# Kernel optimization log

Hardware: AMD Instinct MI355X
Metric: run time of the kernel (lower is better)

## Reference

```python
import jax, jax.numpy as jnp
import numpy as np

L, D, H, M, NC = 12, 768, 12, 3072, 1000
P, IMG, C = 16, 224, 3
HD = D // H // 2  # 32: diff-attn head dim (2*H query heads of HD, H value heads of 2*HD)
B = 32
N = (IMG // P) ** 2 + 1  # 197
EPS = 1e-5


def _layernorm(x, s, b):
    mu = x.mean(-1, keepdims=True)
    var = ((x - mu) ** 2).mean(-1, keepdims=True)
    return (x - mu) * jax.lax.rsqrt(var + EPS) * s + b


def _rmsnorm(x, s):
    ms = (x * x).mean(-1, keepdims=True)
    return x * jax.lax.rsqrt(ms + EPS) * s


def _diff_attn(x, qw, kw, vw, ow, lq1, lk1, lq2, lk2, sls, lam_init):
    b, n, _ = x.shape
    q = (x @ qw).reshape(b, n, 2 * H, HD)
    k = (x @ kw).reshape(b, n, 2 * H, HD)
    v = (x @ vw).reshape(b, n, H, 2 * HD)
    scores = jnp.einsum('bnhd,bmhd->bhnm', q, k) * (HD ** -0.5)
    attn = jax.nn.softmax(scores, axis=-1)  # [b, 2H, n, n]
    lam = jnp.exp(jnp.sum(lq1 * lk1)) - jnp.exp(jnp.sum(lq2 * lk2)) + lam_init
    attn = attn.reshape(b, H, 2, n, n)
    attn = attn[:, :, 0] - lam * attn[:, :, 1]  # differential attention map
    out = jnp.einsum('bhnm,bmhd->bnhd', attn, v)  # [b, n, H, 2*HD]
    out = _rmsnorm(out, sls) * (1.0 - lam_init)
    return out.reshape(b, n, D) @ ow


def _forward(x, conv_w, conv_b, cls_token, pos_emb,
             ln1_s, ln1_b, q_w, k_w, v_w, o_w, lq1, lk1, lq2, lk2, subln_s,
             ln2_s, ln2_b, w1, b1, w2, b2, lnf_s, lnf_b, head_w, head_b):
    # patch embed: conv stride=patch, then flatten to tokens
    h = jax.lax.conv_general_dilated(x, conv_w, (P, P), 'VALID',
                                     dimension_numbers=('NCHW', 'OIHW', 'NCHW'))
    h = h + conv_b[None, :, None, None]
    bsz = x.shape[0]
    h = h.reshape(bsz, D, -1).transpose(0, 2, 1)  # [B, 196, D]
    h = jnp.concatenate([jnp.broadcast_to(cls_token, (bsz, 1, D)), h], axis=1)
    h = h + pos_emb
    for i in range(L):
        lam_init = 0.8 - 0.6 * np.exp(-0.3 * i)
        a = _diff_attn(_layernorm(h, ln1_s[i], ln1_b[i]), q_w[i], k_w[i], v_w[i], o_w[i],
                       lq1[i], lk1[i], lq2[i], lk2[i], subln_s[i], lam_init)
        h = h + a
        m = _layernorm(h, ln2_s[i], ln2_b[i])
        m = jax.nn.gelu(m @ w1[i] + b1[i]) @ w2[i] + b2[i]
        h = h + m
    h = _layernorm(h, lnf_s, lnf_b)
    return h[:, 0] @ head_w + head_b


def setup_inputs() -> dict:
    key = jax.random.key(0)
    ks = iter(jax.random.split(key, 40))
    def rn(shape, s=0.02):
        return jax.random.normal(next(ks), shape, jnp.float32) * s
    return {
        'x': jax.random.normal(next(ks), (B, C, IMG, IMG), jnp.float32),
        'conv_w': rn((D, C, P, P)), 'conv_b': jnp.zeros((D,), jnp.float32),
        'cls_token': jnp.zeros((1, 1, D), jnp.float32),
        'pos_emb': rn((1, N, D)),
        'ln1_s': jnp.ones((L, D), jnp.float32), 'ln1_b': jnp.zeros((L, D), jnp.float32),
        'q_w': rn((L, D, D)), 'k_w': rn((L, D, D)), 'v_w': rn((L, D, D)), 'o_w': rn((L, D, D)),
        'lq1': rn((L, HD), 0.1), 'lk1': rn((L, HD), 0.1),
        'lq2': rn((L, HD), 0.1), 'lk2': rn((L, HD), 0.1),
        'subln_s': jnp.ones((L, 2 * HD), jnp.float32),
        'ln2_s': jnp.ones((L, D), jnp.float32), 'ln2_b': jnp.zeros((L, D), jnp.float32),
        'w1': rn((L, D, M)), 'b1': jnp.zeros((L, M), jnp.float32),
        'w2': rn((L, M, D)), 'b2': jnp.zeros((L, D), jnp.float32),
        'lnf_s': jnp.ones((D,), jnp.float32), 'lnf_b': jnp.zeros((D,), jnp.float32),
        'head_w': rn((D, NC)), 'head_b': jnp.zeros((NC,), jnp.float32),
    }


def reference(x, conv_w, conv_b, cls_token, pos_emb,
              ln1_s, ln1_b, q_w, k_w, v_w, o_w, lq1, lk1, lq2, lk2, subln_s,
              ln2_s, ln2_b, w1, b1, w2, b2, lnf_s, lnf_b, head_w, head_b):
    return _forward(x, conv_w, conv_b, cls_token, pos_emb,
                    ln1_s, ln1_b, q_w, k_w, v_w, o_w, lq1, lk1, lq2, lk2, subln_s,
                    ln2_s, ln2_b, w1, b1, w2, b2, lnf_s, lnf_b, head_w, head_b)
```

## Files before the change

kernel.cpp:

```cpp
#include <hip/hip_runtime.h>
#include <cmath>


typedef unsigned short u16;
typedef u16 u16x4 __attribute__((ext_vector_type(4)));
typedef u16 u16x8 __attribute__((ext_vector_type(8)));
typedef float fx4 __attribute__((ext_vector_type(4)));
typedef __bf16 bf16x8 __attribute__((ext_vector_type(8)));

#define MROWS 6304
#define MPAD  6400

#define WAITV(N) asm volatile("s_waitcnt vmcnt(" #N ")" ::: "memory")

__device__ __forceinline__ float bf2f(u16 u) {
  union { unsigned int i; float f; } c; c.i = ((unsigned int)u) << 16; return c.f;
}
__device__ __forceinline__ u16 f2bf(float f) {
  union { float f; unsigned int i; } c; c.f = f;
  return (u16)((c.i + 0x7FFFu + ((c.i >> 16) & 1u)) >> 16);
}
__device__ __forceinline__ float gelu_f(float x) {
  float u = 0.7978845608028654f * (x + 0.044715f * x * x * x);
  u = fminf(fmaxf(u, -30.f), 30.f);
  float e = __expf(2.f * u);
  return 0.5f * x * (1.f + (e - 1.f) / (e + 1.f));
}

__device__ __forceinline__ void gload16(const void* g, void* l) {
  __builtin_amdgcn_global_load_lds(
      (const __attribute__((address_space(1))) void*)g,
      (__attribute__((address_space(3))) void*)l, 16, 0, 0);
}

__device__ __forceinline__ int xcd_swz(int orig, int nwg) {
  int q = nwg >> 3, r = nwg & 7;
  int x = orig & 7, i = orig >> 3;
  return (x < r ? x * (q + 1) : r * (q + 1) + (x - r) * q) + i;
}

enum { EP_F32 = 0, EP_BF16 = 1, EP_GELU_BF16 = 2, EP_RESID_F32 = 3 };

template<int MODE>
__device__ __forceinline__ void ep_store(void* outp, const float* __restrict__ resid,
                                         size_t m, size_t n, size_t N, float v) {
  if (MODE == EP_GELU_BF16)      ((u16*)outp)[m * N + n] = f2bf(gelu_f(v));
  else if (MODE == EP_BF16)      ((u16*)outp)[m * N + n] = f2bf(v);
  else if (MODE == EP_RESID_F32) ((float*)outp)[m * N + n] = resid[m * N + n] + v;
  else                           ((float*)outp)[m * N + n] = v;
}

template<int MODE, bool BIAS>
__device__ __forceinline__
void gemm_big_body(const u16* __restrict__ A, const u16* __restrict__ Bt,
                   const float* __restrict__ bias, const float* __restrict__ resid,
                   void* __restrict__ outp, int M, int N, int K, int NT)
{
  __shared__ unsigned char lds[2][2 * 128 * 64 * 2];
  const int tid = threadIdx.x;
  const int lane = tid & 63, w = tid >> 6;
  const int g = lane >> 4, l = lane & 15;
  const int wr = w >> 1, wc = w & 1;
  const int wg = xcd_swz(blockIdx.x, gridDim.x);
  const int bm = (wg / NT) * 128, bn = (wg % NT) * 128;

  const int swz_half = ((lane & 7) ^ ((lane >> 3) & 7)) << 3;
  const int srow = 32 * w + (lane >> 3);
  const u16* gA = A + (size_t)(bm + srow) * K + swz_half;
  const u16* gB = Bt + (size_t)(bn + srow) * K + swz_half;

  fx4 acc[4][4] = {};

  auto STAGE = [&](int buf, int kt) {
    unsigned char* bA = &lds[buf][0] + 4096 * w;
    unsigned char* bB = bA + 16384;
    #pragma unroll
    for (int c = 0; c < 4; ++c) {
      gload16(gA + (size_t)(8 * c) * K + kt, bA + (8 * c) * 128);
      gload16(gB + (size_t)(8 * c) * K + kt, bB + (8 * c) * 128);
    }
  };

  STAGE(0, 0);
  int cur = 0;
  for (int kt = 0; kt < K; kt += 64) {
    if (kt + 64 < K) {
      STAGE(cur ^ 1, kt + 64);
      WAITV(8);
    } else {
      WAITV(0);
    }
    __builtin_amdgcn_s_barrier();
    __builtin_amdgcn_sched_barrier(0);
    const unsigned char* As = &lds[cur][0];
    const unsigned char* Bs = As + 16384;
    #pragma unroll
    for (int kk = 0; kk < 2; ++kk) {
      bf16x8 af[4], bfr[4];
      #pragma unroll
      for (int i = 0; i < 4; ++i) {
        int ar = wr * 64 + i * 16 + l;
        af[i] = *(const bf16x8*)(As + ar * 128 + ((kk * 64 + g * 16) ^ ((ar & 7) << 4)));
        int br = wc * 64 + i * 16 + l;
        bfr[i] = *(const bf16x8*)(Bs + br * 128 + ((kk * 64 + g * 16) ^ ((br & 7) << 4)));
      }
      #pragma unroll
      for (int i = 0; i < 4; ++i)
        #pragma unroll
        for (int j = 0; j < 4; ++j)
          acc[i][j] = __builtin_amdgcn_mfma_f32_16x16x32_bf16(af[i], bfr[j], acc[i][j], 0, 0, 0);
    }
    __builtin_amdgcn_sched_barrier(0);
    __builtin_amdgcn_s_barrier();
    cur ^= 1;
  }
  #pragma unroll
  for (int j = 0; j < 4; ++j) {
    int n = bn + wc * 64 + j * 16 + l;
    float bv = BIAS ? bias[n] : 0.f;
    #pragma unroll
    for (int i = 0; i < 4; ++i) {
      int mbase = bm + wr * 64 + i * 16 + g * 4;
      #pragma unroll
      for (int q = 0; q < 4; ++q) {
        int m = mbase + q;
        if (m < M) ep_store<MODE>(outp, resid, m, n, N, acc[i][j][q] + bv);
      }
    }
  }
}

template<int MODE, bool BIAS>
__device__ __forceinline__
void gemm_n64_body(const u16* __restrict__ A, const u16* __restrict__ Bt,
                   const float* __restrict__ bias, const float* __restrict__ resid,
                   void* __restrict__ outp, int M, int N, int K, int NT)
{
  __shared__ unsigned char lds[2][(128 + 64) * 64 * 2];
  const int tid = threadIdx.x;
  const int lane = tid & 63, w = tid >> 6;
  const int g = lane >> 4, l = lane & 15;
  const int wg = xcd_swz(blockIdx.x, gridDim.x);
  const int bm = (wg / NT) * 128, bn = (wg % NT) * 64;

  const int swz_half = ((lane & 7) ^ ((lane >> 3) & 7)) << 3;
  const u16* gA = A + (size_t)(bm + 32 * w + (lane >> 3)) * K + swz_half;
  const u16* gB = Bt + (size_t)(bn + 16 * w + (lane >> 3)) * K + swz_half;

  fx4 acc[2][4] = {};

  auto STAGE = [&](int buf, int kt) {
    unsigned char* bA = &lds[buf][0] + 4096 * w;
    unsigned char* bB = &lds[buf][0] + 16384 + 2048 * w;
    #pragma unroll
    for (int c = 0; c < 4; ++c)
      gload16(gA + (size_t)(8 * c) * K + kt, bA + (8 * c) * 128);
    #pragma unroll
    for (int c = 0; c < 2; ++c)
      gload16(gB + (size_t)(8 * c) * K + kt, bB + (8 * c) * 128);
  };

  STAGE(0, 0);
  int cur = 0;
  for (int kt = 0; kt < K; kt += 64) {
    if (kt + 64 < K) {
      STAGE(cur ^ 1, kt + 64);
      WAITV(6);
    } else {
      WAITV(0);
    }
    __builtin_amdgcn_s_barrier();
    __builtin_amdgcn_sched_barrier(0);
    const unsigned char* As = &lds[cur][0];
    const unsigned char* Bs = As + 16384;
    #pragma unroll
    for (int kk = 0; kk < 2; ++kk) {
      bf16x8 af[2], bfr[4];
      #pragma unroll
      for (int i = 0; i < 2; ++i) {
        int ar = w * 32 + i * 16 + l;
        af[i] = *(const bf16x8*)(As + ar * 128 + ((kk * 64 + g * 16) ^ ((ar & 7) << 4)));
      }
      #pragma unroll
      for (int j = 0; j < 4; ++j) {
        int br = j * 16 + l;
        bfr[j] = *(const bf16x8*)(Bs + br * 128 + ((kk * 64 + g * 16) ^ ((br & 7) << 4)));
      }
      #pragma unroll
      for (int i = 0; i < 2; ++i)
        #pragma unroll
        for (int j = 0; j < 4; ++j)
          acc[i][j] = __builtin_amdgcn_mfma_f32_16x16x32_bf16(af[i], bfr[j], acc[i][j], 0, 0, 0);
    }
    __builtin_amdgcn_sched_barrier(0);
    __builtin_amdgcn_s_barrier();
    cur ^= 1;
  }
  #pragma unroll
  for (int j = 0; j < 4; ++j) {
    int n = bn + j * 16 + l;
    float bv = BIAS ? bias[n] : 0.f;
    #pragma unroll
    for (int i = 0; i < 2; ++i) {
      int mbase = bm + w * 32 + i * 16 + g * 4;
      #pragma unroll
      for (int q = 0; q < 4; ++q) {
        int m = mbase + q;
        if (m < M) ep_store<MODE>(outp, resid, m, n, N, acc[i][j][q] + bv);
      }
    }
  }
}

__global__ __launch_bounds__(256) void patch_gemm(const u16* A, const u16* Bt, float* outp) {
  gemm_n64_body<EP_F32, false>(A, Bt, nullptr, nullptr, outp, 6272, 768, 768, 12);
}
__global__ __launch_bounds__(256) void qkv_gemm(const u16* A, const u16* Bt, u16* outp) {
  gemm_big_body<EP_BF16, false>(A, Bt, nullptr, nullptr, outp, MROWS, 2304, 768, 18);
}
__global__ __launch_bounds__(256) void oproj_gemm(const u16* A, const u16* Bt,
                                                  const float* resid, float* outp) {
  gemm_n64_body<EP_RESID_F32, false>(A, Bt, nullptr, resid, outp, MROWS, 768, 768, 12);
}
__global__ __launch_bounds__(256) void mlp1_gemm(const u16* A, const u16* Bt,
                                                 const float* bias, u16* outp) {
  gemm_big_body<EP_GELU_BF16, true>(A, Bt, bias, nullptr, outp, MROWS, 3072, 768, 24);
}
__global__ __launch_bounds__(256) void mlp2_gemm(const u16* A, const u16* Bt,
                                                 const float* bias, const float* resid,
                                                 float* outp) {
  gemm_n64_body<EP_RESID_F32, true>(A, Bt, bias, resid, outp, MROWS, 768, 3072, 12);
}

template<bool OUTF32>
__global__ __launch_bounds__(64)
void layernorm_k(const float* __restrict__ x, const float* __restrict__ s,
                 const float* __restrict__ b, void* __restrict__ outp, size_t in_rstride)
{
  int r = blockIdx.x, lane = threadIdx.x;
  const fx4* xp = (const fx4*)(x + (size_t)r * in_rstride);
  fx4 v[3];
  float sum = 0.f, sq = 0.f;
  #pragma unroll
  for (int j = 0; j < 3; ++j) {
    v[j] = xp[j * 64 + lane];
    #pragma unroll
    for (int e = 0; e < 4; ++e) { sum += v[j][e]; sq += v[j][e] * v[j][e]; }
  }
  #pragma unroll
  for (int off = 32; off; off >>= 1) { sum += __shfl_xor(sum, off); sq += __shfl_xor(sq, off); }
  float mu = sum * (1.f / 768.f);
  float var = sq * (1.f / 768.f) - mu * mu;
  float rs = rsqrtf(var + 1e-5f);
  const fx4* sp = (const fx4*)s;
  const fx4* bp = (const fx4*)b;
  #pragma unroll
  for (int j = 0; j < 3; ++j) {
    fx4 sv = sp[j * 64 + lane], bv = bp[j * 64 + lane];
    if (OUTF32) {
      fx4 o;
      #pragma unroll
      for (int e = 0; e < 4; ++e) o[e] = (v[j][e] - mu) * rs * sv[e] + bv[e];
      *(fx4*)((float*)outp + (size_t)r * 768 + (j * 64 + lane) * 4) = o;
    } else {
      u16x4 o;
      #pragma unroll
      for (int e = 0; e < 4; ++e) o[e] = f2bf((v[j][e] - mu) * rs * sv[e] + bv[e]);
      *(u16x4*)((u16*)outp + (size_t)r * 768 + (j * 64 + lane) * 4) = o;
    }
  }
}

#define KSTR 40
#define VSTR 232
#define DA_LDS (2 * 224 * KSTR * 2 + 64 * VSTR * 2 + 4 * 16 * VSTR * 2)

__global__ __launch_bounds__(256)
void diff_attn(const u16* __restrict__ qkv, const float* __restrict__ lam_p,
               const float* __restrict__ sls, u16* __restrict__ outp, float lam_init)
{
  extern __shared__ char smem[];
  u16* K1s = (u16*)smem;
  u16* K2s = K1s + 224 * KSTR;
  u16* Vt  = K2s + 224 * KSTR;
  const int tid = threadIdx.x;
  const int w = tid >> 6, lane = tid & 63;
  const int g = lane >> 4, l = lane & 15;
  u16* Pw = Vt + 64 * VSTR + w * 16 * VSTR;

  const int bh = blockIdx.x;
  const int b = bh / 12, hh = bh % 12;
  const u16* base = qkv + (size_t)b * 197 * 2304;

  if (tid < 197) {
    const u16* kr = base + (size_t)tid * 2304 + 768 + hh * 64;
    *(u16x8*)(K1s + tid * KSTR + 0)  = *(const u16x8*)(kr + 0);
    *(u16x8*)(K1s + tid * KSTR + 8)  = *(const u16x8*)(kr + 8);
    *(u16x8*)(K1s + tid * KSTR + 16) = *(const u16x8*)(kr + 16);
    *(u16x8*)(K1s + tid * KSTR + 24) = *(const u16x8*)(kr + 24);
    *(u16x8*)(K2s + tid * KSTR + 0)  = *(const u16x8*)(kr + 32);
    *(u16x8*)(K2s + tid * KSTR + 8)  = *(const u16x8*)(kr + 40);
    *(u16x8*)(K2s + tid * KSTR + 16) = *(const u16x8*)(kr + 48);
    *(u16x8*)(K2s + tid * KSTR + 24) = *(const u16x8*)(kr + 56);
    const u16* vr = base + (size_t)tid * 2304 + 1536 + hh * 64;
    #pragma unroll
    for (int jj = 0; jj < 8; ++jj) {
      u16x8 vv = *(const u16x8*)(vr + jj * 8);
      #pragma unroll
      for (int e = 0; e < 8; ++e) Vt[(jj * 8 + e) * VSTR + tid] = vv[e];
    }
  }
  for (int idx = tid; idx < 64 * 27; idx += 256) {
    Vt[(idx / 27) * VSTR + 197 + (idx % 27)] = 0;
  }
  __syncthreads();

  const float lam = lam_p[0];
  const float oscale = 1.f - lam_init;
  const float scale = 0.17677669529663687f;
  const fx4 zero = {};

  for (int qb = w; qb < 13; qb += 4) {
    const int qbase = qb * 16;
    const u16* qrow = base + (size_t)(qbase + l) * 2304 + hh * 64;
    bf16x8 qf1 = *(const bf16x8*)(qrow + g * 8);
    bf16x8 qf2 = *(const bf16x8*)(qrow + 32 + g * 8);

    fx4 s1[14], s2[14];
    #pragma unroll
    for (int t = 0; t < 14; ++t) {
      bf16x8 kf1 = *(const bf16x8*)(K1s + (t * 16 + l) * KSTR + g * 8);
      bf16x8 kf2 = *(const bf16x8*)(K2s + (t * 16 + l) * KSTR + g * 8);
      s1[t] = __builtin_amdgcn_mfma_f32_16x16x32_bf16(qf1, kf1, zero, 0, 0, 0);
      s2[t] = __builtin_amdgcn_mfma_f32_16x16x32_bf16(qf2, kf2, zero, 0, 0, 0);
    }

    float mx1[4] = {-1e30f, -1e30f, -1e30f, -1e30f};
    float mx2[4] = {-1e30f, -1e30f, -1e30f, -1e30f};
    #pragma unroll
    for (int t = 0; t < 14; ++t) {
      bool ok = (t * 16 + l) < 197;
      #pragma unroll
      for (int q = 0; q < 4; ++q) {
        float v1 = ok ? s1[t][q] * scale : -1e30f;
        float v2 = ok ? s2[t][q] * scale : -1e30f;
        s1[t][q] = v1; s2[t][q] = v2;
        mx1[q] = fmaxf(mx1[q], v1); mx2[q] = fmaxf(mx2[q], v2);
      }
    }
    #pragma unroll
    for (int off = 8; off; off >>= 1)
      #pragma unroll
      for (int q = 0; q < 4; ++q) {
        mx1[q] = fmaxf(mx1[q], __shfl_xor(mx1[q], off));
        mx2[q] = fmaxf(mx2[q], __shfl_xor(mx2[q], off));
      }
    float z1[4] = {0, 0, 0, 0}, z2[4] = {0, 0, 0, 0};
    #pragma unroll
    for (int t = 0; t < 14; ++t)
      #pragma unroll
      for (int q = 0; q < 4; ++q) {
        float p1 = __expf(s1[t][q] - mx1[q]);
        float p2 = __expf(s2[t][q] - mx2[q]);
        s1[t][q] = p1; s2[t][q] = p2;
        z1[q] += p1; z2[q] += p2;
      }
    #pragma unroll
    for (int off = 8; off; off >>= 1)
      #pragma unroll
      for (int q = 0; q < 4; ++q) {
        z1[q] += __shfl_xor(z1[q], off);
        z2[q] += __shfl_xor(z2[q], off);
      }
    float r1[4], r2[4];
    #pragma unroll
    for (int q = 0; q < 4; ++q) { r1[q] = 1.f / z1[q]; r2[q] = lam / z2[q]; }

    #pragma unroll
    for (int t = 0; t < 14; ++t)
      #pragma unroll
      for (int q = 0; q < 4; ++q) {
        float pc = s1[t][q] * r1[q] - s2[t][q] * r2[q];
        Pw[(g * 4 + q) * VSTR + t * 16 + l] = f2bf(pc);
      }

    fx4 o[4] = {};
    #pragma unroll
    for (int mt = 0; mt < 7; ++mt) {
      bf16x8 pa = *(const bf16x8*)(Pw + l * VSTR + mt * 32 + g * 8);
      #pragma unroll
      for (int j = 0; j < 4; ++j) {
        bf16x8 vb = *(const bf16x8*)(Vt + (j * 16 + l) * VSTR + mt * 32 + g * 8);
        o[j] = __builtin_amdgcn_mfma_f32_16x16x32_bf16(pa, vb, o[j], 0, 0, 0);
      }
    }

    float ms[4] = {0, 0, 0, 0};
    #pragma unroll
    for (int j = 0; j < 4; ++j)
      #pragma unroll
      for (int q = 0; q < 4; ++q) ms[q] += o[j][q] * o[j][q];
    #pragma unroll
    for (int off = 8; off; off >>= 1)
      #pragma unroll
      for (int q = 0; q < 4; ++q) ms[q] += __shfl_xor(ms[q], off);
    float rr[4];
    #pragma unroll
    for (int q = 0; q < 4; ++q) rr[q] = rsqrtf(ms[q] * (1.f / 64.f) + 1e-5f) * oscale;
    #pragma unroll
    for (int j = 0; j < 4; ++j) {
      float slv = sls[j * 16 + l];
      #pragma unroll
      for (int q = 0; q < 4; ++q) {
        int row = qbase + g * 4 + q;
        if (row < 197)
          outp[(size_t)(b * 197 + row) * 768 + hh * 64 + j * 16 + l] = f2bf(o[j][q] * rr[q] * slv);
      }
    }
  }
}

__global__ __launch_bounds__(256)
void prep_weights(const float* __restrict__ qw, const float* __restrict__ kw,
                  const float* __restrict__ vw, const float* __restrict__ ow,
                  const float* __restrict__ w1, const float* __restrict__ w2,
                  u16* __restrict__ qkvt, u16* __restrict__ ot,
                  u16* __restrict__ w1t, u16* __restrict__ w2t,
                  const float* __restrict__ lq1, const float* __restrict__ lk1,
                  const float* __restrict__ lq2, const float* __restrict__ lk2,
                  float* __restrict__ lam_out, float lam_init)
{
  int bid = blockIdx.x;
  if (bid == 1728) {
    if (threadIdx.x < 64) {
      int lane = threadIdx.x;
      float p1 = lane < 32 ? lq1[lane] * lk1[lane] : 0.f;
      float p2 = lane < 32 ? lq2[lane] * lk2[lane] : 0.f;
      #pragma unroll
      for (int off = 32; off; off >>= 1) { p1 += __shfl_xor(p1, off); p2 += __shfl_xor(p2, off); }
      if (lane == 0) lam_out[0] = __expf(p1) - __expf(p2) + lam_init;
    }
    return;
  }
  const float* src; u16* dst; int Kd, Nd, tx, ty;
  if (bid < 576) {
    int which = bid / 144, t = bid % 144;
    ty = t / 12; tx = t % 12; Kd = 768; Nd = 768;
    src = (which == 0) ? qw : (which == 1) ? kw : (which == 2) ? vw : ow;
    dst = (which < 3) ? (qkvt + (size_t)which * 768 * 768) : ot;
  } else if (bid < 1152) {
    int t = bid - 576; ty = t / 12; tx = t % 12; Kd = 768; Nd = 3072; src = w1; dst = w1t;
  } else {
    int t = bid - 1152; ty = t / 48; tx = t % 48; Kd = 3072; Nd = 768; src = w2; dst = w2t;
  }
  __shared__ u16 tile[64][65];
  int tid2 = threadIdx.x;
  int k0 = tx * 64, n0 = ty * 64;
  #pragma unroll
  for (int j = 0; j < 16; ++j) {
    int idx = j * 256 + tid2;
    int rr = idx >> 6, cc = idx & 63;
    tile[rr][cc] = f2bf(src[(size_t)(k0 + rr) * Nd + n0 + cc]);
  }
  __syncthreads();
  #pragma unroll
  for (int j = 0; j < 16; ++j) {
    int idx = j * 256 + tid2;
    int rr = idx >> 6, cc = idx & 63;
    dst[(size_t)(n0 + rr) * Kd + k0 + cc] = tile[cc][rr];
  }
}

__global__ void convert_cw(const float* __restrict__ src, u16* __restrict__ dst)
{
  int i4 = blockIdx.x * 256 + threadIdx.x;
  fx4 v = *(const fx4*)(src + (size_t)i4 * 4);
  u16x4 o;
  #pragma unroll
  for (int e = 0; e < 4; ++e) o[e] = f2bf(v[e]);
  *(u16x4*)(dst + (size_t)i4 * 4) = o;
}

__global__ void im2col(const float* __restrict__ x, u16* __restrict__ A0)
{
  int i4 = blockIdx.x * 256 + threadIdx.x;
  int base = i4 * 4;
  int r = base / 768, c0 = base % 768;
  int b = r / 196, p = r % 196;
  int py = p / 14, px = p % 14;
  int ch = c0 >> 8;
  int cc = c0 & 255;
  int iy = cc >> 4, ix = cc & 15;
  const float* src = x + (((size_t)(b * 3 + ch) * 224 + py * 16 + iy) * 224 + px * 16 + ix);
  fx4 v = *(const fx4*)src;
  u16x4 o;
  #pragma unroll
  for (int e = 0; e < 4; ++e) o[e] = f2bf(v[e]);
  *(u16x4*)(A0 + base) = o;
}

__global__ void assemble(const float* __restrict__ tmp, const float* __restrict__ conv_b,
                         const float* __restrict__ cls, const float* __restrict__ pos,
                         float* __restrict__ h)
{
  int i4 = blockIdx.x * 256 + threadIdx.x;
  int base = i4 * 4;
  int r = base / 768, d = base % 768;
  int b = r / 197, n = r % 197;
  fx4 pv = *(const fx4*)(pos + (size_t)n * 768 + d);
  fx4 v;
  if (n == 0) {
    v = *(const fx4*)(cls + d);
  } else {
    v = *(const fx4*)(tmp + (size_t)(b * 196 + n - 1) * 768 + d);
    fx4 cb = *(const fx4*)(conv_b + d);
    v = v + cb;
  }
  *(fx4*)(h + (size_t)r * 768 + d) = v + pv;
}

__global__ __launch_bounds__(256)
void head_kernel(const float* __restrict__ ln, const float* __restrict__ hw,
                 const float* __restrict__ hb, float* __restrict__ outp)
{
  int r = blockIdx.x;
  int c = blockIdx.y * 256 + threadIdx.x;
  if (c >= 1000) return;
  const float* lr = ln + (size_t)r * 768;
  float acc = hb[c];
  for (int d = 0; d < 768; ++d)
    acc = fmaf(lr[d], hw[(size_t)d * 1000 + c], acc);
  outp[r * 1000 + c] = acc;
}

extern "C" void kernel_launch(void* const* d_in, const int* in_sizes, int n_in,
                              void* d_out, int out_size, void* d_ws, size_t ws_size,
                              hipStream_t stream)
{
  (void)in_sizes; (void)n_in; (void)out_size; (void)ws_size;
  const float* x      = (const float*)d_in[0];
  const float* conv_w = (const float*)d_in[1];
  const float* conv_b = (const float*)d_in[2];
  const float* cls    = (const float*)d_in[3];
  const float* pos    = (const float*)d_in[4];
  const float* ln1_s  = (const float*)d_in[5];
  const float* ln1_b  = (const float*)d_in[6];
  const float* q_w    = (const float*)d_in[7];
  const float* k_w    = (const float*)d_in[8];
  const float* v_w    = (const float*)d_in[9];
  const float* o_w    = (const float*)d_in[10];
  const float* lq1    = (const float*)d_in[11];
  const float* lk1    = (const float*)d_in[12];
  const float* lq2    = (const float*)d_in[13];
  const float* lk2    = (const float*)d_in[14];
  const float* slsx   = (const float*)d_in[15];
  const float* ln2_s  = (const float*)d_in[16];
  const float* ln2_b  = (const float*)d_in[17];
  const float* w1     = (const float*)d_in[18];
  const float* b1     = (const float*)d_in[19];
  const float* w2     = (const float*)d_in[20];
  const float* b2     = (const float*)d_in[21];
  const float* lnf_s  = (const float*)d_in[22];
  const float* lnf_b  = (const float*)d_in[23];
  const float* head_w = (const float*)d_in[24];
  const float* head_b = (const float*)d_in[25];
  float* out = (float*)d_out;

  char* ws = (char*)d_ws;
  size_t off = 0;
  auto alloc = [&](size_t bytes) { size_t p = off; off += (bytes + 255) & ~(size_t)255; return p; };
  u16*   A_bf  = (u16*)  (ws + alloc((size_t)MPAD * 768 * 2));
  u16*   big   = (u16*)  (ws + alloc((size_t)MPAD * 3072 * 2));
  float* h     = (float*)(ws + alloc((size_t)MROWS * 768 * 4));
  u16*   wqkv  = (u16*)  (ws + alloc((size_t)2304 * 768 * 2));
  u16*   wo    = (u16*)  (ws + alloc((size_t)768 * 768 * 2));
  u16*   w1t   = (u16*)  (ws + alloc((size_t)3072 * 768 * 2));
  u16*   w2t   = (u16*)  (ws + alloc((size_t)768 * 3072 * 2));
  float* lnf_o = (float*)(ws + alloc((size_t)32 * 768 * 4));
  float* lam   = (float*)(ws + alloc(256));
  float* convtmp = (float*)big;
  u16*   cwbf  = w1t;

  hipFuncSetAttribute((const void*)diff_attn,
                      hipFuncAttributeMaxDynamicSharedMemorySize, DA_LDS);

  convert_cw<<<576, 256, 0, stream>>>(conv_w, cwbf);
  im2col<<<4704, 256, 0, stream>>>(x, A_bf);
  patch_gemm<<<588, 256, 0, stream>>>(A_bf, cwbf, convtmp);
  assemble<<<4728, 256, 0, stream>>>(convtmp, conv_b, cls, pos, h);

  for (int l = 0; l < 12; ++l) {
    float lam_init = 0.8f - 0.6f * expf(-0.3f * (float)l);
    prep_weights<<<1729, 256, 0, stream>>>(
        q_w + (size_t)l * 589824, k_w + (size_t)l * 589824,
        v_w + (size_t)l * 589824, o_w + (size_t)l * 589824,
        w1 + (size_t)l * 2359296, w2 + (size_t)l * 2359296,
        wqkv, wo, w1t, w2t,
        lq1 + l * 32, lk1 + l * 32, lq2 + l * 32, lk2 + l * 32,
        lam, lam_init);
    layernorm_k<false><<<MROWS, 64, 0, stream>>>(h, ln1_s + l * 768, ln1_b + l * 768, A_bf, (size_t)768);
    qkv_gemm<<<900, 256, 0, stream>>>(A_bf, wqkv, big);
    diff_attn<<<384, 256, DA_LDS, stream>>>(big, lam, slsx + l * 64, A_bf, lam_init);
    oproj_gemm<<<600, 256, 0, stream>>>(A_bf, wo, h, h);
    layernorm_k<false><<<MROWS, 64, 0, stream>>>(h, ln2_s + l * 768, ln2_b + l * 768, A_bf, (size_t)768);
    mlp1_gemm<<<1200, 256, 0, stream>>>(A_bf, w1t, b1 + l * 3072, big);
    mlp2_gemm<<<600, 256, 0, stream>>>(big, w2t, b2 + l * 768, h, h);
  }

  layernorm_k<true><<<32, 64, 0, stream>>>(h, lnf_s, lnf_b, lnf_o, (size_t)197 * 768);
  head_kernel<<<dim3(32, 4), 256, 0, stream>>>(lnf_o, head_w, head_b, out);
}
```

Measured before the change: 3.118 ms.

## Use 256x256 tiles with 8-wave four-phase pipelined GEMM for QKV and MLP1

Replaces the 128x128, 4-wave GEMM body used by the QKV and MLP1 projections with a 256x256 tile, 512-thread kernel that uses 128 KB of dynamic LDS. The K loop is split into four quadrant phases that interleave global-to-LDS staging of the next tiles with MFMA work, using barriers and s_setprio. The aim is more operand reuse per LDS byte and better overlap of loads with compute. In exchange the grids become much smaller (225 and 300 blocks), so the 256-CU device will see wave-quantization and tail effects, and each block holds more registers per wave.

```diff
diff --git a/kernel.cpp b/kernel.cpp
--- a/kernel.cpp
+++ b/kernel.cpp
@@ -52,82 +52,99 @@
 
 template<int MODE, bool BIAS>
 __device__ __forceinline__
-void gemm_big_body(const u16* __restrict__ A, const u16* __restrict__ Bt,
+void gemm_256_body(const u16* __restrict__ A, const u16* __restrict__ Bt,
                    const float* __restrict__ bias, const float* __restrict__ resid,
                    void* __restrict__ outp, int M, int N, int K, int NT)
 {
-  __shared__ unsigned char lds[2][2 * 128 * 64 * 2];
+  extern __shared__ unsigned char lds[];
   const int tid = threadIdx.x;
   const int lane = tid & 63, w = tid >> 6;
   const int g = lane >> 4, l = lane & 15;
-  const int wr = w >> 1, wc = w & 1;
+  const int wr = w >> 2, wc = w & 3;
   const int wg = xcd_swz(blockIdx.x, gridDim.x);
-  const int bm = (wg / NT) * 128, bn = (wg % NT) * 128;
-
-  const int swz_half = ((lane & 7) ^ ((lane >> 3) & 7)) << 3;
-  const int srow = 32 * w + (lane >> 3);
-  const u16* gA = A + (size_t)(bm + srow) * K + swz_half;
-  const u16* gB = Bt + (size_t)(bn + srow) * K + swz_half;
-
-  fx4 acc[4][4] = {};
-
-  auto STAGE = [&](int buf, int kt) {
-    unsigned char* bA = &lds[buf][0] + 4096 * w;
-    unsigned char* bB = bA + 16384;
-    #pragma unroll
-    for (int c = 0; c < 4; ++c) {
-      gload16(gA + (size_t)(8 * c) * K + kt, bA + (8 * c) * 128);
-      gload16(gB + (size_t)(8 * c) * K + kt, bB + (8 * c) * 128);
-    }
+  const int bm = (wg / NT) * 256, bn = (wg % NT) * 256;
+  const int NKT = K >> 6;
+
+  const int srow = w * 16 + (lane >> 3);
+  const int scol = ((lane & 7) ^ ((lane >> 3) & 7)) << 3;
+  const u16* gA = A + (size_t)bm * K + scol;
+  const u16* gB = Bt + (size_t)bn * K + scol;
+  const int ldso = (w * 16) * 128;
+
+  auto STG = [&](int buf, int op, int half, int t) {
+    const u16* src = (op ? gB : gA) + (size_t)(half * 128 + srow) * K + t * 64;
+    unsigned char* d = lds + buf * 65536 + op * 32768 + half * 16384 + ldso;
+    gload16(src, d);
+    gload16(src + (size_t)8 * K, d + 1024);
   };
 
-  STAGE(0, 0);
-  int cur = 0;
-  for (int kt = 0; kt < K; kt += 64) {
-    if (kt + 64 < K) {
-      STAGE(cur ^ 1, kt + 64);
-      WAITV(8);
-    } else {
-      WAITV(0);
-    }
-    __builtin_amdgcn_s_barrier();
-    __builtin_amdgcn_sched_barrier(0);
-    const unsigned char* As = &lds[cur][0];
-    const unsigned char* Bs = As + 16384;
-    #pragma unroll
-    for (int kk = 0; kk < 2; ++kk) {
-      bf16x8 af[4], bfr[4];
-      #pragma unroll
-      for (int i = 0; i < 4; ++i) {
-        int ar = wr * 64 + i * 16 + l;
-        af[i] = *(const bf16x8*)(As + ar * 128 + ((kk * 64 + g * 16) ^ ((ar & 7) << 4)));
-        int br = wc * 64 + i * 16 + l;
-        bfr[i] = *(const bf16x8*)(Bs + br * 128 + ((kk * 64 + g * 16) ^ ((br & 7) << 4)));
-      }
-      #pragma unroll
-      for (int i = 0; i < 4; ++i)
-        #pragma unroll
-        for (int j = 0; j < 4; ++j)
-          acc[i][j] = __builtin_amdgcn_mfma_f32_16x16x32_bf16(af[i], bfr[j], acc[i][j], 0, 0, 0);
-    }
-    __builtin_amdgcn_sched_barrier(0);
-    __builtin_amdgcn_s_barrier();
-    cur ^= 1;
-  }
-  #pragma unroll
-  for (int j = 0; j < 4; ++j) {
-    int n = bn + wc * 64 + j * 16 + l;
-    float bv = BIAS ? bias[n] : 0.f;
-    #pragma unroll
-    for (int i = 0; i < 4; ++i) {
-      int mbase = bm + wr * 64 + i * 16 + g * 4;
-      #pragma unroll
-      for (int q = 0; q < 4; ++q) {
-        int m = mbase + q;
-        if (m < M) ep_store<MODE>(outp, resid, m, n, N, acc[i][j][q] + bv);
-      }
-    }
-  }
+  fx4 acc[2][2][4][2] = {};
+
+  STG(0, 0, 0, 0); STG(0, 1, 0, 0); STG(0, 0, 1, 0); STG(0, 1, 1, 0);
+  STG(1, 0, 0, 1); STG(1, 1, 0, 1);
+  WAITV(4);
+  __builtin_amdgcn_s_barrier();
+
+  for (int T = 0; T < NKT; ++T) {
+    const unsigned char* Ab = lds + (T & 1) * 65536;
+    const unsigned char* Bb = Ab + 32768;
+
+#define RD_A(i2, kk, mh) (*(const bf16x8*)(Ab + ((mh)*128 + wr*64 + (i2)*16 + l)*128 + (((kk)*64 + g*16) ^ ((l & 7) << 4))))
+#define RD_B(j2, kk, nh) (*(const bf16x8*)(Bb + ((nh)*128 + wc*32 + (j2)*16 + l)*128 + (((kk)*64 + g*16) ^ ((l & 7) << 4))))
+#define PHASE(mh, nh, DOWAIT, ...)                                             \
+    {                                                                          \
+      bf16x8 af0[4], af1[4], bq0[2], bq1[2];                                   \
+      _Pragma("unroll") for (int i2 = 0; i2 < 4; ++i2) {                       \
+        af0[i2] = RD_A(i2, 0, mh); af1[i2] = RD_A(i2, 1, mh);                  \
+      }                                                                        \
+      _Pragma("unroll") for (int j2 = 0; j2 < 2; ++j2) {                       \
+        bq0[j2] = RD_B(j2, 0, nh); bq1[j2] = RD_B(j2, 1, nh);                  \
+      }                                                                        \
+      __VA_ARGS__;                                                             \
+      if (DOWAIT) WAITV(4);                                                    \
+      __builtin_amdgcn_s_barrier();                                            \
+      asm volatile("s_waitcnt lgkmcnt(0)" ::: "memory");                       \
+      __builtin_amdgcn_sched_barrier(0);                                       \
+      __builtin_amdgcn_s_setprio(1);                                           \
+      _Pragma("unroll") for (int i2 = 0; i2 < 4; ++i2)                         \
+        _Pragma("unroll") for (int j2 = 0; j2 < 2; ++j2) {                     \
+          acc[mh][nh][i2][j2] = __builtin_amdgcn_mfma_f32_16x16x32_bf16(       \
+              af0[i2], bq0[j2], acc[mh][nh][i2][j2], 0, 0, 0);                 \
+          acc[mh][nh][i2][j2] = __builtin_amdgcn_mfma_f32_16x16x32_bf16(       \
+              af1[i2], bq1[j2], acc[mh][nh][i2][j2], 0, 0, 0);                 \
+        }                                                                      \
+      __builtin_amdgcn_s_setprio(0);                                           \
+      __builtin_amdgcn_s_barrier();                                            \
+    }
+
+    PHASE(0, 0, false, { if (T + 1 < NKT) STG((T + 1) & 1, 0, 1, T + 1); })
+    PHASE(0, 1, false, { if (T + 1 < NKT) STG((T + 1) & 1, 1, 1, T + 1); })
+    PHASE(1, 0, false, { if (T + 2 < NKT) STG(T & 1, 0, 0, T + 2); })
+    PHASE(1, 1, true,  { if (T + 2 < NKT) STG(T & 1, 1, 0, T + 2); })
+
+#undef PHASE
+#undef RD_A
+#undef RD_B
+  }
+
+  #pragma unroll
+  for (int mh = 0; mh < 2; ++mh)
+    #pragma unroll
+    for (int i2 = 0; i2 < 4; ++i2)
+      #pragma unroll
+      for (int qr = 0; qr < 4; ++qr) {
+        int m = bm + mh * 128 + wr * 64 + i2 * 16 + g * 4 + qr;
+        if (m < M) {
+          #pragma unroll
+          for (int nh = 0; nh < 2; ++nh)
+            #pragma unroll
+            for (int j2 = 0; j2 < 2; ++j2) {
+              int n = bn + nh * 128 + wc * 32 + j2 * 16 + l;
+              float bv = BIAS ? bias[n] : 0.f;
+              ep_store<MODE>(outp, resid, m, n, N, acc[mh][nh][i2][j2][qr] + bv);
+            }
+        }
+      }
 }
 
 template<int MODE, bool BIAS>
@@ -215,16 +232,16 @@
 __global__ __launch_bounds__(256) void patch_gemm(const u16* A, const u16* Bt, float* outp) {
   gemm_n64_body<EP_F32, false>(A, Bt, nullptr, nullptr, outp, 6272, 768, 768, 12);
 }
-__global__ __launch_bounds__(256) void qkv_gemm(const u16* A, const u16* Bt, u16* outp) {
-  gemm_big_body<EP_BF16, false>(A, Bt, nullptr, nullptr, outp, MROWS, 2304, 768, 18);
+__global__ __launch_bounds__(512) void qkv_gemm(const u16* A, const u16* Bt, u16* outp) {
+  gemm_256_body<EP_BF16, false>(A, Bt, nullptr, nullptr, outp, MROWS, 2304, 768, 9);
 }
 __global__ __launch_bounds__(256) void oproj_gemm(const u16* A, const u16* Bt,
                                                   const float* resid, float* outp) {
   gemm_n64_body<EP_RESID_F32, false>(A, Bt, nullptr, resid, outp, MROWS, 768, 768, 12);
 }
-__global__ __launch_bounds__(256) void mlp1_gemm(const u16* A, const u16* Bt,
+__global__ __launch_bounds__(512) void mlp1_gemm(const u16* A, const u16* Bt,
                                                  const float* bias, u16* outp) {
-  gemm_big_body<EP_GELU_BF16, true>(A, Bt, bias, nullptr, outp, MROWS, 3072, 768, 24);
+  gemm_256_body<EP_GELU_BF16, true>(A, Bt, bias, nullptr, outp, MROWS, 3072, 768, 12);
 }
 __global__ __launch_bounds__(256) void mlp2_gemm(const u16* A, const u16* Bt,
                                                  const float* bias, const float* resid,
@@ -583,6 +600,10 @@
 
   hipFuncSetAttribute((const void*)diff_attn,
                       hipFuncAttributeMaxDynamicSharedMemorySize, DA_LDS);
+  hipFuncSetAttribute((const void*)qkv_gemm,
+                      hipFuncAttributeMaxDynamicSharedMemorySize, 131072);
+  hipFuncSetAttribute((const void*)mlp1_gemm,
+                      hipFuncAttributeMaxDynamicSharedMemorySize, 131072);
 
   convert_cw<<<576, 256, 0, stream>>>(conv_w, cwbf);
   im2col<<<4704, 256, 0, stream>>>(x, A_bf);
@@ -599,11 +620,11 @@
         lq1 + l * 32, lk1 + l * 32, lq2 + l * 32, lk2 + l * 32,
         lam, lam_init);
     layernorm_k<false><<<MROWS, 64, 0, stream>>>(h, ln1_s + l * 768, ln1_b + l * 768, A_bf, (size_t)768);
-    qkv_gemm<<<900, 256, 0, stream>>>(A_bf, wqkv, big);
+    qkv_gemm<<<225, 512, 131072, stream>>>(A_bf, wqkv, big);
     diff_attn<<<384, 256, DA_LDS, stream>>>(big, lam, slsx + l * 64, A_bf, lam_init);
     oproj_gemm<<<600, 256, 0, stream>>>(A_bf, wo, h, h);
     layernorm_k<false><<<MROWS, 64, 0, stream>>>(h, ln2_s + l * 768, ln2_b + l * 768, A_bf, (size_t)768);
-    mlp1_gemm<<<1200, 256, 0, stream>>>(A_bf, w1t, b1 + l * 3072, big);
+    mlp1_gemm<<<300, 512, 131072, stream>>>(A_bf, w1t, b1 + l * 3072, big);
     mlp2_gemm<<<600, 256, 0, stream>>>(big, w2t, b2 + l * 768, h, h);
   }
 
```

Measured after the change: 3.136 ms. Within noise of the previous version (+0.6%).
